# Optimization experiments

Hardware: AMD Instinct MI355X
Metric: run time of the kernel (lower is better)

Reference implementation:

```python
import jax, jax.numpy as jnp
import numpy as np

MAX_LEN = 960
EMB = 200
SQRT_DK = np.sqrt(MAX_LEN).astype(np.float32)  # note: sqrt(max_len), as in source


def setup_inputs() -> dict:
    key = jax.random.key(0)
    k1, k2, k3, k4 = jax.random.split(key, 4)
    B, S, F = 16, 2048, 800
    x = jax.random.normal(k1, (B, S, F), dtype=jnp.float32)
    # torch Linear(960,200) weight init scale ~ 1/sqrt(960); random normal scaled
    scale = 1.0 / np.sqrt(MAX_LEN)
    Wq = jax.random.normal(k2, (MAX_LEN, EMB), dtype=jnp.float32) * scale
    Wk = jax.random.normal(k3, (MAX_LEN, EMB), dtype=jnp.float32) * scale
    Wv = jax.random.normal(k4, (MAX_LEN, EMB), dtype=jnp.float32) * scale
    return {"x": x, "Wq": Wq, "Wk": Wk, "Wv": Wv}


def reference(x, Wq, Wk, Wv):
    # pad feature dim up to MAX_LEN with zeros
    pad = MAX_LEN - x.shape[2]
    x = jnp.pad(x, ((0, 0), (0, 0), (0, pad)))
    gelu = lambda t: jax.nn.gelu(t, approximate=False)  # torch nn.GELU default = exact
    q = gelu(jnp.einsum('bsf,fe->bse', x, Wq))  # [B,S,E]
    k = gelu(jnp.einsum('bsf,fe->bse', x, Wk))
    v = gelu(jnp.einsum('bsf,fe->bse', x, Wv))
    score = jnp.einsum('bqe,bke->bqk', q, k) / SQRT_DK  # [B,S,S]
    attn = jax.nn.softmax(score, axis=-1)
    return jnp.einsum('bqk,bke->bqe', attn, v)  # [B,S,E]
```

## Files before the change

kernel.cpp:

```cpp
#include <hip/hip_runtime.h>
#include <hip/hip_bf16.h>

#define B_  16
#define S_  2048
#define F_  800
#define E_  200
#define EP  224
#define KP  832
#define KSP 256
#define M_  (B_ * S_)

typedef __attribute__((ext_vector_type(8))) short short8;
typedef __attribute__((ext_vector_type(4))) float f32x4;

#define QSCL (0.03227486121839514f * 1.4426950408889634f)

__device__ __forceinline__ unsigned short f2bf(float f) {
    __hip_bfloat16 h = __float2bfloat16(f);
    return *reinterpret_cast<unsigned short*>(&h);
}

__device__ __forceinline__ float exp2_fast(float x) {
    float r;
    asm("v_exp_f32 %0, %1" : "=v"(r) : "v"(x));
    return r;
}

__device__ __forceinline__ float rcp_fast(float x) {
    float r;
    asm("v_rcp_f32 %0, %1" : "=v"(r) : "v"(x));
    return r;
}

__device__ __forceinline__ float gelu_fast(float x) {
    const float i = x + 0.044715f * x * x * x;
    const float z = 2.302265314f * i;
    return x * rcp_fast(1.0f + exp2_fast(-z));
}

__device__ __forceinline__ void gload_lds16(const void* g, void* l) {
    __builtin_amdgcn_global_load_lds(
        (const __attribute__((address_space(1))) unsigned int*)g,
        (__attribute__((address_space(3))) unsigned int*)l, 16, 0, 0);
}

__global__ __launch_bounds__(256)
void prep_x(const float* __restrict__ x, unsigned short* __restrict__ xb) {
    const int id = blockIdx.x * 256 + threadIdx.x;
    const int r  = id / (KP / 8);
    const int c8 = id % (KP / 8);
    ushort4 lo = {0, 0, 0, 0}, hi = {0, 0, 0, 0};
    if (c8 < F_ / 8) {
        const float4 a = *reinterpret_cast<const float4*>(x + (size_t)r * F_ + c8 * 8);
        const float4 b = *reinterpret_cast<const float4*>(x + (size_t)r * F_ + c8 * 8 + 4);
        lo.x = f2bf(a.x); lo.y = f2bf(a.y); lo.z = f2bf(a.z); lo.w = f2bf(a.w);
        hi.x = f2bf(b.x); hi.y = f2bf(b.y); hi.z = f2bf(b.z); hi.w = f2bf(b.w);
    }
    unsigned short* dst = xb + (size_t)r * KP + c8 * 8;
    *reinterpret_cast<ushort4*>(dst) = lo;
    *reinterpret_cast<ushort4*>(dst + 4) = hi;
}

__global__ __launch_bounds__(256)
void prep_w(const float* __restrict__ Wq, const float* __restrict__ Wk,
            const float* __restrict__ Wv, unsigned short* __restrict__ wt) {
    const int id = blockIdx.x * 256 + threadIdx.x;
    const int sel = id / (EP * KP);
    const int rem = id % (EP * KP);
    const int e = rem / KP;
    const int k = rem % KP;
    const float* W = (sel == 0) ? Wq : ((sel == 1) ? Wk : Wv);
    float v = (e < E_ && k < F_) ? W[(size_t)k * E_ + e] : 0.0f;
    wt[id] = f2bf(v);
}

#define STAGE(XB, WB, KK) do {                                                   \
    const int k0s = (KK) * 32;                                                   \
    _Pragma("unroll")                                                            \
    for (int i = 0; i < 2; ++i) {                                                \
        const int j = w * 2 + i;                                                 \
        const int row = 16 * j + rS;                                             \
        gload_lds16(xb + (size_t)(m0 + row) * KP + k0s + ((pS ^ (row & 3)) * 8), \
                    &XB[j * 512]);                                               \
    }                                                                            \
    _Pragma("unroll")                                                            \
    for (int i = 0; i < 4; ++i) {                                                \
        const int j = i * 4 + w;                                                 \
        if (j < 14) {                                                            \
            const int row = 16 * j + rS;                                         \
            gload_lds16(wsel + (size_t)row * KP + k0s + ((pS ^ (row & 3)) * 8),  \
                        &WB[j * 512]);                                           \
        }                                                                        \
    }                                                                            \
} while (0)

#define COMPUTE(XB, WB) do {                                                     \
    short8 afr[4];                                                               \
    _Pragma("unroll")                                                            \
    for (int rf = 0; rf < 4; ++rf) {                                             \
        const int row = wr * 64 + rf * 16 + ln15;                                \
        afr[rf] = *reinterpret_cast<const short8*>(                              \
            &XB[row * 32 + ((g ^ (row & 3)) * 8)]);                              \
    }                                                                            \
    _Pragma("unroll")                                                            \
    for (int cf = 0; cf < 7; ++cf) {                                             \
        const int row = wc * 112 + cf * 16 + ln15;                               \
        short8 bfr = *reinterpret_cast<const short8*>(                           \
            &WB[row * 32 + ((g ^ (row & 3)) * 8)]);                              \
        _Pragma("unroll")                                                        \
        for (int rf = 0; rf < 4; ++rf)                                           \
            acc[rf][cf] = __builtin_amdgcn_mfma_f32_16x16x32_bf16(               \
                afr[rf], bfr, acc[rf][cf], 0, 0, 0);                             \
    }                                                                            \
} while (0)

__global__ __launch_bounds__(256, 2)
void gemm_qkv(const unsigned short* __restrict__ xb,
              const unsigned short* __restrict__ wt,
              unsigned short* __restrict__ qbuf,
              unsigned short* __restrict__ kbuf,
              unsigned short* __restrict__ vtbuf) {
    const int sel = blockIdx.y;
    const int m0 = blockIdx.x * 128;
    const int t = threadIdx.x;
    const int lane = t & 63;
    const int w = t >> 6;
    const int wr = w >> 1;
    const int wc = w & 1;
    const int ln15 = lane & 15;
    const int g = lane >> 4;

    __shared__ __align__(16) unsigned short X0s[128 * 32];
    __shared__ __align__(16) unsigned short W0s[224 * 32];
    __shared__ __align__(16) unsigned short X1s[128 * 32];
    __shared__ __align__(16) unsigned short W1s[224 * 32];

    const unsigned short* wsel = wt + (size_t)sel * EP * KP;

    f32x4 acc[4][7];
#pragma unroll
    for (int i = 0; i < 4; ++i)
#pragma unroll
        for (int j = 0; j < 7; ++j) acc[i][j] = (f32x4)0.0f;

    const int rS = lane >> 2;
    const int pS = lane & 3;

    STAGE(X0s, W0s, 0);
    __syncthreads();
#pragma unroll
    for (int p = 0; p < 12; ++p) {
        STAGE(X1s, W1s, 2 * p + 1);
        COMPUTE(X0s, W0s);
        __syncthreads();
        STAGE(X0s, W0s, 2 * p + 2);
        COMPUTE(X1s, W1s);
        __syncthreads();
    }
    STAGE(X1s, W1s, 25);
    COMPUTE(X0s, W0s);
    __syncthreads();
    COMPUTE(X1s, W1s);

#pragma unroll
    for (int rf = 0; rf < 4; ++rf) {
        const int row = m0 + wr * 64 + rf * 16 + g * 4;
#pragma unroll
        for (int cf = 0; cf < 7; ++cf) {
            const int col = wc * 112 + cf * 16 + ln15;
            if (sel == 0) {
#pragma unroll
                for (int tt = 0; tt < 4; ++tt)
                    qbuf[(size_t)(row + tt) * EP + col] =
                        f2bf(gelu_fast(acc[rf][cf][tt]) * QSCL);
            } else if (sel == 1) {
#pragma unroll
                for (int tt = 0; tt < 4; ++tt)
                    kbuf[(size_t)(row + tt) * KSP + col] = f2bf(gelu_fast(acc[rf][cf][tt]));
            } else {
                const int bb = row >> 11, s = row & 2047;
                ushort4 pk;
                if (col == 200) {
                    pk.x = 0x3F80; pk.y = 0x3F80; pk.z = 0x3F80; pk.w = 0x3F80;
                } else {
                    pk.x = f2bf(gelu_fast(acc[rf][cf][0]));
                    pk.y = f2bf(gelu_fast(acc[rf][cf][1]));
                    pk.z = f2bf(gelu_fast(acc[rf][cf][2]));
                    pk.w = f2bf(gelu_fast(acc[rf][cf][3]));
                }
                *reinterpret_cast<ushort4*>(
                    &vtbuf[((size_t)(bb * EP + col)) * S_ + s]) = pk;
            }
        }
    }
}

#define BQ  128
#define BKV 64

#define ASTAGE(KB, VB, KT) do {                                                  \
    const int kv0s = (KT) * BKV;                                                 \
    {                                                                            \
        const int r_in = lane >> 5;                                              \
        const int p = lane & 31;                                                 \
        _Pragma("unroll")                                                        \
        for (int i = 0; i < 8; ++i) {                                            \
            const int j = w * 8 + i;                                             \
            const int row = 2 * j + r_in;                                        \
            gload_lds16(kb_b + (size_t)(kv0s + row) * KSP + ((p ^ (row & 7)) * 8),\
                        &KB[j * 512]);                                           \
        }                                                                        \
    }                                                                            \
    {                                                                            \
        const int r_in = lane >> 3;                                              \
        const int p = lane & 7;                                                  \
        _Pragma("unroll")                                                        \
        for (int i = 0; i < 7; ++i) {                                            \
            const int j = w * 7 + i;                                             \
            const int row = 8 * j + r_in;                                        \
            gload_lds16(vt_b + (size_t)row * S_ + kv0s + ((p ^ (row & 7)) * 8),  \
                        &VB[j * 512]);                                           \
        }                                                                        \
    }                                                                            \
} while (0)

#define ACOMPUTE(KB, VB) do {                                                    \
    _Pragma("unroll")                                                            \
    for (int rf = 0; rf < 2; ++rf) {                                             \
        f32x4 sacc[4];                                                           \
        _Pragma("unroll")                                                        \
        for (int n = 0; n < 4; ++n) {                                            \
            f32x4 a = (f32x4)0.0f;                                               \
            const int krow = n * 16 + ln15;                                      \
            const unsigned short* kr = &KB[krow * KSP];                          \
            const int rx = krow & 7;                                             \
            _Pragma("unroll")                                                    \
            for (int s = 0; s < 7; ++s) {                                        \
                short8 bf = *reinterpret_cast<const short8*>(                    \
                    kr + (((s * 4 + g) ^ rx) * 8));                              \
                a = __builtin_amdgcn_mfma_f32_16x16x32_bf16(qf[rf][s], bf, a, 0, 0, 0); \
            }                                                                    \
            sacc[n] = a;                                                         \
        }                                                                        \
        _Pragma("unroll")                                                        \
        for (int n = 0; n < 4; ++n)                                              \
            _Pragma("unroll")                                                    \
            for (int tt = 0; tt < 4; ++tt)                                       \
                Plds[w][rf * 16 + g * 4 + tt][n * 16 + ln15] =                   \
                    f2bf(exp2_fast(sacc[n][tt]));                                \
    }                                                                            \
    short8 pf[2][2];                                                             \
    _Pragma("unroll")                                                            \
    for (int rf = 0; rf < 2; ++rf) {                                             \
        pf[rf][0] = *reinterpret_cast<const short8*>(&Plds[w][rf * 16 + ln15][g * 8]); \
        pf[rf][1] = *reinterpret_cast<const short8*>(&Plds[w][rf * 16 + ln15][32 + g * 8]); \
    }                                                                            \
    _Pragma("unroll")                                                            \
    for (int n = 0; n < 14; ++n) {                                               \
        const int vrow = n * 16 + ln15;                                          \
        const unsigned short* vr = &VB[vrow * 64];                               \
        const int rx = vrow & 7;                                                 \
        short8 b0 = *reinterpret_cast<const short8*>(vr + ((g ^ rx) * 8));       \
        short8 b1 = *reinterpret_cast<const short8*>(vr + (((4 + g) ^ rx) * 8)); \
        _Pragma("unroll")                                                        \
        for (int rf = 0; rf < 2; ++rf) {                                         \
            o[rf][n] = __builtin_amdgcn_mfma_f32_16x16x32_bf16(pf[rf][0], b0, o[rf][n], 0, 0, 0); \
            o[rf][n] = __builtin_amdgcn_mfma_f32_16x16x32_bf16(pf[rf][1], b1, o[rf][n], 0, 0, 0); \
        }                                                                        \
    }                                                                            \
} while (0)

__global__ __launch_bounds__(256, 1)
void attn_kernel(const unsigned short* __restrict__ qbuf,
                 const unsigned short* __restrict__ kbuf,
                 const unsigned short* __restrict__ vtbuf,
                 float* __restrict__ out) {
    const int id = blockIdx.x;
    const int slot = id >> 3;
    const int b = 2 * (id & 7) + (slot >> 4);
    const int q0 = (slot & 15) * BQ;
    const int t = threadIdx.x;
    const int lane = t & 63;
    const int w = t >> 6;
    const int ln15 = lane & 15;
    const int g = lane >> 4;

    __shared__ __align__(16) unsigned short Ks[2][BKV * KSP];
    __shared__ __align__(16) unsigned short Vts[2][EP * 64];
    __shared__ __align__(16) unsigned short Plds[4][32][68];

    short8 qf[2][7];
#pragma unroll
    for (int rf = 0; rf < 2; ++rf) {
        const unsigned short* qp =
            qbuf + (size_t)(b * S_ + q0 + w * 32 + rf * 16 + ln15) * EP + g * 8;
#pragma unroll
        for (int s = 0; s < 7; ++s)
            qf[rf][s] = *reinterpret_cast<const short8*>(qp + s * 32);
    }

    f32x4 o[2][14];
#pragma unroll
    for (int rf = 0; rf < 2; ++rf)
#pragma unroll
        for (int i = 0; i < 14; ++i) o[rf][i] = (f32x4)0.0f;

    const unsigned short* kb_b = kbuf + (size_t)b * S_ * KSP;
    const unsigned short* vt_b = vtbuf + (size_t)b * EP * S_;

    ASTAGE(Ks[0], Vts[0], 0);
    __syncthreads();
    for (int kt = 0; kt < S_ / BKV - 1; ++kt) {
        const int cur = kt & 1;
        ASTAGE(Ks[cur ^ 1], Vts[cur ^ 1], kt + 1);
        ACOMPUTE(Ks[cur], Vts[cur]);
        __syncthreads();
    }
    ACOMPUTE(Ks[1], Vts[1]);

#pragma unroll
    for (int rf = 0; rf < 2; ++rf) {
        float l[4];
#pragma unroll
        for (int tt = 0; tt < 4; ++tt)
            l[tt] = __shfl(o[rf][12][tt], (lane & 48) + 8, 64);
#pragma unroll
        for (int tt = 0; tt < 4; ++tt) {
            const float inv = 1.0f / l[tt];
            const int row = q0 + w * 32 + rf * 16 + g * 4 + tt;
            float* op = out + (size_t)(b * S_ + row) * E_;
#pragma unroll
            for (int n = 0; n < 13; ++n) {
                const int e = n * 16 + ln15;
                if (e < E_) op[e] = o[rf][n][tt] * inv;
            }
        }
    }
}

extern "C" void kernel_launch(void* const* d_in, const int* in_sizes, int n_in,
                              void* d_out, int out_size, void* d_ws, size_t ws_size,
                              hipStream_t stream) {
    const float* x  = (const float*)d_in[0];
    const float* Wq = (const float*)d_in[1];
    const float* Wk = (const float*)d_in[2];
    const float* Wv = (const float*)d_in[3];
    float* out = (float*)d_out;

    unsigned short* xb    = (unsigned short*)d_ws;
    unsigned short* wt    = xb + (size_t)M_ * KP;
    unsigned short* qbuf  = wt + (size_t)3 * EP * KP;
    unsigned short* kbuf  = qbuf + (size_t)M_ * EP;
    unsigned short* vtbuf = kbuf + (size_t)M_ * KSP;

    prep_x<<<dim3(M_ * (KP / 8) / 256), 256, 0, stream>>>(x, xb);
    prep_w<<<dim3(3 * EP * KP / 256), 256, 0, stream>>>(Wq, Wk, Wv, wt);
    gemm_qkv<<<dim3(256, 3), 256, 0, stream>>>(xb, wt, qbuf, kbuf, vtbuf);
    attn_kernel<<<dim3(256), 256, 0, stream>>>(qbuf, kbuf, vtbuf, out);
}
```

Measured before the change: 188.4 us.

## Split attention block across 8 waves with 16 query rows each

The attention kernel now launches 512 threads (8 waves) per block instead of 256. Each wave owns 16 query rows rather than 32, which halves the per-wave Q fragments and output accumulators. The K/V staging loads are redistributed across the 8 waves, with a guard for the 28 V chunks. Each K/V tile loaded into LDS is now shared by more waves and register pressure drops, in exchange for the extra cost of synchronising twice as many waves. Launch bounds are raised to (512, 2), but the LDS footprint probably still limits the CU to one block.

```diff
diff --git a/kernel.cpp b/kernel.cpp
--- a/kernel.cpp
+++ b/kernel.cpp
@@ -200,61 +200,55 @@
 
 #define ASTAGE(KB, VB, KT) do {                                                  \
     const int kv0s = (KT) * BKV;                                                 \
-    {                                                                            \
+    {                            \
         const int r_in = lane >> 5;                                              \
         const int p = lane & 31;                                                 \
         _Pragma("unroll")                                                        \
-        for (int i = 0; i < 8; ++i) {                                            \
-            const int j = w * 8 + i;                                             \
+        for (int i = 0; i < 4; ++i) {                                            \
+            const int j = w * 4 + i;                                             \
             const int row = 2 * j + r_in;                                        \
             gload_lds16(kb_b + (size_t)(kv0s + row) * KSP + ((p ^ (row & 7)) * 8),\
                         &KB[j * 512]);                                           \
         }                                                                        \
     }                                                                            \
-    {                                                                            \
+    {                                        \
         const int r_in = lane >> 3;                                              \
         const int p = lane & 7;                                                  \
         _Pragma("unroll")                                                        \
-        for (int i = 0; i < 7; ++i) {                                            \
-            const int j = w * 7 + i;                                             \
-            const int row = 8 * j + r_in;                                        \
-            gload_lds16(vt_b + (size_t)row * S_ + kv0s + ((p ^ (row & 7)) * 8),  \
-                        &VB[j * 512]);                                           \
+        for (int i = 0; i < 4; ++i) {                                            \
+            const int j = i * 8 + w;                                             \
+            if (j < 28) {                                                        \
+                const int row = 8 * j + r_in;                                    \
+                gload_lds16(vt_b + (size_t)row * S_ + kv0s + ((p ^ (row & 7)) * 8),\
+                            &VB[j * 512]);                                       \
+            }                                                                    \
         }                                                                        \
     }                                                                            \
 } while (0)
 
 #define ACOMPUTE(KB, VB) do {                                                    \
-    _Pragma("unroll")                                                            \
-    for (int rf = 0; rf < 2; ++rf) {                                             \
-        f32x4 sacc[4];                                                           \
-        _Pragma("unroll")                                                        \
-        for (int n = 0; n < 4; ++n) {                                            \
-            f32x4 a = (f32x4)0.0f;                                               \
-            const int krow = n * 16 + ln15;                                      \
-            const unsigned short* kr = &KB[krow * KSP];                          \
-            const int rx = krow & 7;                                             \
-            _Pragma("unroll")                                                    \
-            for (int s = 0; s < 7; ++s) {                                        \
-                short8 bf = *reinterpret_cast<const short8*>(                    \
-                    kr + (((s * 4 + g) ^ rx) * 8));                              \
-                a = __builtin_amdgcn_mfma_f32_16x16x32_bf16(qf[rf][s], bf, a, 0, 0, 0); \
-            }                                                                    \
-            sacc[n] = a;                                                         \
+    f32x4 sacc[4];                                                               \
+    _Pragma("unroll")                                                            \
+    for (int n = 0; n < 4; ++n) {                                                \
+        f32x4 a = (f32x4)0.0f;                                                   \
+        const int krow = n * 16 + ln15;                                          \
+        const unsigned short* kr = &KB[krow * KSP];                              \
+        const int rx = krow & 7;                                                 \
+        _Pragma("unroll")                                                        \
+        for (int s = 0; s < 7; ++s) {                                            \
+            short8 bf = *reinterpret_cast<const short8*>(                        \
+                kr + (((s * 4 + g) ^ rx) * 8));                                  \
+            a = __builtin_amdgcn_mfma_f32_16x16x32_bf16(qf[s], bf, a, 0, 0, 0);  \
         }                                                                        \
-        _Pragma("unroll")                                                        \
-        for (int n = 0; n < 4; ++n)                                              \
-            _Pragma("unroll")                                                    \
-            for (int tt = 0; tt < 4; ++tt)                                       \
-                Plds[w][rf * 16 + g * 4 + tt][n * 16 + ln15] =                   \
-                    f2bf(exp2_fast(sacc[n][tt]));                                \
-    }                                                                            \
-    short8 pf[2][2];                                                             \
-    _Pragma("unroll")                                                            \
-    for (int rf = 0; rf < 2; ++rf) {                                             \
-        pf[rf][0] = *reinterpret_cast<const short8*>(&Plds[w][rf * 16 + ln15][g * 8]); \
-        pf[rf][1] = *reinterpret_cast<const short8*>(&Plds[w][rf * 16 + ln15][32 + g * 8]); \
-    }                                                                            \
+        sacc[n] = a;                                                             \
+    }                                                                            \
+    _Pragma("unroll")                                                            \
+    for (int n = 0; n < 4; ++n)                                                  \
+        _Pragma("unroll")                                                        \
+        for (int tt = 0; tt < 4; ++tt)                                           \
+            Plds[w][g * 4 + tt][n * 16 + ln15] = f2bf(exp2_fast(sacc[n][tt]));   \
+    short8 pf0 = *reinterpret_cast<const short8*>(&Plds[w][ln15][g * 8]);        \
+    short8 pf1 = *reinterpret_cast<const short8*>(&Plds[w][ln15][32 + g * 8]);   \
     _Pragma("unroll")                                                            \
     for (int n = 0; n < 14; ++n) {                                               \
         const int vrow = n * 16 + ln15;                                          \
@@ -262,15 +256,12 @@
         const int rx = vrow & 7;                                                 \
         short8 b0 = *reinterpret_cast<const short8*>(vr + ((g ^ rx) * 8));       \
         short8 b1 = *reinterpret_cast<const short8*>(vr + (((4 + g) ^ rx) * 8)); \
-        _Pragma("unroll")                                                        \
-        for (int rf = 0; rf < 2; ++rf) {                                         \
-            o[rf][n] = __builtin_amdgcn_mfma_f32_16x16x32_bf16(pf[rf][0], b0, o[rf][n], 0, 0, 0); \
-            o[rf][n] = __builtin_amdgcn_mfma_f32_16x16x32_bf16(pf[rf][1], b1, o[rf][n], 0, 0, 0); \
-        }                                                                        \
+        o[n] = __builtin_amdgcn_mfma_f32_16x16x32_bf16(pf0, b0, o[n], 0, 0, 0);  \
+        o[n] = __builtin_amdgcn_mfma_f32_16x16x32_bf16(pf1, b1, o[n], 0, 0, 0);  \
     }                                                                            \
 } while (0)
 
-__global__ __launch_bounds__(256, 1)
+__global__ __launch_bounds__(512, 2)
 void attn_kernel(const unsigned short* __restrict__ qbuf,
                  const unsigned short* __restrict__ kbuf,
                  const unsigned short* __restrict__ vtbuf,
@@ -287,23 +278,20 @@
 
     __shared__ __align__(16) unsigned short Ks[2][BKV * KSP];
     __shared__ __align__(16) unsigned short Vts[2][EP * 64];
-    __shared__ __align__(16) unsigned short Plds[4][32][68];
-
-    short8 qf[2][7];
-#pragma unroll
-    for (int rf = 0; rf < 2; ++rf) {
+    __shared__ __align__(16) unsigned short Plds[8][16][68];
+
+    short8 qf[7];
+    {
         const unsigned short* qp =
-            qbuf + (size_t)(b * S_ + q0 + w * 32 + rf * 16 + ln15) * EP + g * 8;
+            qbuf + (size_t)(b * S_ + q0 + w * 16 + ln15) * EP + g * 8;
 #pragma unroll
         for (int s = 0; s < 7; ++s)
-            qf[rf][s] = *reinterpret_cast<const short8*>(qp + s * 32);
-    }
-
-    f32x4 o[2][14];
-#pragma unroll
-    for (int rf = 0; rf < 2; ++rf)
-#pragma unroll
-        for (int i = 0; i < 14; ++i) o[rf][i] = (f32x4)0.0f;
+            qf[s] = *reinterpret_cast<const short8*>(qp + s * 32);
+    }
+
+    f32x4 o[14];
+#pragma unroll
+    for (int i = 0; i < 14; ++i) o[i] = (f32x4)0.0f;
 
     const unsigned short* kb_b = kbuf + (size_t)b * S_ * KSP;
     const unsigned short* vt_b = vtbuf + (size_t)b * EP * S_;
@@ -318,21 +306,20 @@
     }
     ACOMPUTE(Ks[1], Vts[1]);
 
-#pragma unroll
-    for (int rf = 0; rf < 2; ++rf) {
+    {
         float l[4];
 #pragma unroll
         for (int tt = 0; tt < 4; ++tt)
-            l[tt] = __shfl(o[rf][12][tt], (lane & 48) + 8, 64);
+            l[tt] = __shfl(o[12][tt], (lane & 48) + 8, 64);
 #pragma unroll
         for (int tt = 0; tt < 4; ++tt) {
             const float inv = 1.0f / l[tt];
-            const int row = q0 + w * 32 + rf * 16 + g * 4 + tt;
+            const int row = q0 + w * 16 + g * 4 + tt;
             float* op = out + (size_t)(b * S_ + row) * E_;
 #pragma unroll
             for (int n = 0; n < 13; ++n) {
                 const int e = n * 16 + ln15;
-                if (e < E_) op[e] = o[rf][n][tt] * inv;
+                if (e < E_) op[e] = o[n][tt] * inv;
             }
         }
     }
@@ -356,5 +343,5 @@
     prep_x<<<dim3(M_ * (KP / 8) / 256), 256, 0, stream>>>(x, xb);
     prep_w<<<dim3(3 * EP * KP / 256), 256, 0, stream>>>(Wq, Wk, Wv, wt);
     gemm_qkv<<<dim3(256, 3), 256, 0, stream>>>(xb, wt, qbuf, kbuf, vtbuf);
-    attn_kernel<<<dim3(256), 256, 0, stream>>>(qbuf, kbuf, vtbuf, out);
-}
+    attn_kernel<<<dim3(256), 512, 0, stream>>>(qbuf, kbuf, vtbuf, out);
+}
```

Result: faster. 170.0 us (-9.8%).

## Split attention output dim across two blocks and compute denominator via MFMA ones

Applied to the files above, without the earlier changes.

The attention kernel now splits the 224-wide value/output dimension into two halves handled by separate blocks, doubling the grid to 512 blocks so more CUs have work. The KV tile shrinks to 32 and the softmax denominator is accumulated with an MFMA against a ones vector instead of being read from the padded ones column. The cost is that QK^T and exp are recomputed in both halves, roughly doubling score work, while the smaller per-block working set and LDS footprint may improve occupancy and load balance.

```diff
diff --git a/kernel.cpp b/kernel.cpp
--- a/kernel.cpp
+++ b/kernel.cpp
@@ -196,40 +196,44 @@
 }
 
 #define BQ  128
-#define BKV 64
+#define BKV 32
 
 #define ASTAGE(KB, VB, KT) do {                                                  \
     const int kv0s = (KT) * BKV;                                                 \
-    {                                                                            \
+    {              \
         const int r_in = lane >> 5;                                              \
         const int p = lane & 31;                                                 \
         _Pragma("unroll")                                                        \
-        for (int i = 0; i < 8; ++i) {                                            \
-            const int j = w * 8 + i;                                             \
+        for (int i = 0; i < 4; ++i) {                                            \
+            const int j = w * 4 + i;                                             \
             const int row = 2 * j + r_in;                                        \
             gload_lds16(kb_b + (size_t)(kv0s + row) * KSP + ((p ^ (row & 7)) * 8),\
                         &KB[j * 512]);                                           \
         }                                                                        \
     }                                                                            \
-    {                                                                            \
-        const int r_in = lane >> 3;                                              \
-        const int p = lane & 7;                                                  \
-        _Pragma("unroll")                                                        \
-        for (int i = 0; i < 7; ++i) {                                            \
-            const int j = w * 7 + i;                                             \
-            const int row = 8 * j + r_in;                                        \
-            gload_lds16(vt_b + (size_t)row * S_ + kv0s + ((p ^ (row & 7)) * 8),  \
-                        &VB[j * 512]);                                           \
+    {             \
+        const int r_in = lane >> 2;                                              \
+        const int p = lane & 3;                                                  \
+        _Pragma("unroll")                                                        \
+        for (int i = 0; i < 2; ++i) {                                            \
+            const int j = i * 4 + w;                                             \
+            if (j < 7) {                                                         \
+                const int lr = 16 * j + r_in;                                    \
+                gload_lds16(vt_b + (size_t)(ehBase + lr) * S_ + kv0s +           \
+                                ((p ^ (lr & 3)) * 8),                            \
+                            &VB[j * 512]);                                       \
+            }                                                                    \
         }                                                                        \
     }                                                                            \
 } while (0)
 
 #define ACOMPUTE(KB, VB) do {                                                    \
+    short8 pf[2];                                                                \
     _Pragma("unroll")                                                            \
     for (int rf = 0; rf < 2; ++rf) {                                             \
-        f32x4 sacc[4];                                                           \
-        _Pragma("unroll")                                                        \
-        for (int n = 0; n < 4; ++n) {                                            \
+        f32x4 sacc[2];                                                           \
+        _Pragma("unroll")                                                        \
+        for (int n = 0; n < 2; ++n) {                                            \
             f32x4 a = (f32x4)0.0f;                                               \
             const int krow = n * 16 + ln15;                                      \
             const unsigned short* kr = &KB[krow * KSP];                          \
@@ -243,30 +247,22 @@
             sacc[n] = a;                                                         \
         }                                                                        \
         _Pragma("unroll")                                                        \
-        for (int n = 0; n < 4; ++n)                                              \
+        for (int n = 0; n < 2; ++n)                                              \
             _Pragma("unroll")                                                    \
             for (int tt = 0; tt < 4; ++tt)                                       \
                 Plds[w][rf * 16 + g * 4 + tt][n * 16 + ln15] =                   \
                     f2bf(exp2_fast(sacc[n][tt]));                                \
-    }                                                                            \
-    short8 pf[2][2];                                                             \
-    _Pragma("unroll")                                                            \
-    for (int rf = 0; rf < 2; ++rf) {                                             \
-        pf[rf][0] = *reinterpret_cast<const short8*>(&Plds[w][rf * 16 + ln15][g * 8]); \
-        pf[rf][1] = *reinterpret_cast<const short8*>(&Plds[w][rf * 16 + ln15][32 + g * 8]); \
-    }                                                                            \
-    _Pragma("unroll")                                                            \
-    for (int n = 0; n < 14; ++n) {                                               \
-        const int vrow = n * 16 + ln15;                                          \
-        const unsigned short* vr = &VB[vrow * 64];                               \
-        const int rx = vrow & 7;                                                 \
-        short8 b0 = *reinterpret_cast<const short8*>(vr + ((g ^ rx) * 8));       \
-        short8 b1 = *reinterpret_cast<const short8*>(vr + (((4 + g) ^ rx) * 8)); \
-        _Pragma("unroll")                                                        \
-        for (int rf = 0; rf < 2; ++rf) {                                         \
-            o[rf][n] = __builtin_amdgcn_mfma_f32_16x16x32_bf16(pf[rf][0], b0, o[rf][n], 0, 0, 0); \
-            o[rf][n] = __builtin_amdgcn_mfma_f32_16x16x32_bf16(pf[rf][1], b1, o[rf][n], 0, 0, 0); \
-        }                                                                        \
+        pf[rf] = *reinterpret_cast<const short8*>(&Plds[w][rf * 16 + ln15][g * 8]); \
+        dn[rf] = __builtin_amdgcn_mfma_f32_16x16x32_bf16(pf[rf], ones8, dn[rf], 0, 0, 0); \
+    }                                                                            \
+    _Pragma("unroll")                                                            \
+    for (int n = 0; n < 7; ++n) {                                                \
+        const int lr = n * 16 + ln15;                                            \
+        short8 b0 = *reinterpret_cast<const short8*>(                            \
+            &VB[lr * 32 + ((g ^ (lr & 3)) * 8)]);                                \
+        _Pragma("unroll")                                                        \
+        for (int rf = 0; rf < 2; ++rf)                                           \
+            o[rf][n] = __builtin_amdgcn_mfma_f32_16x16x32_bf16(pf[rf], b0, o[rf][n], 0, 0, 0); \
     }                                                                            \
 } while (0)
 
@@ -277,8 +273,11 @@
                  float* __restrict__ out) {
     const int id = blockIdx.x;
     const int slot = id >> 3;
-    const int b = 2 * (id & 7) + (slot >> 4);
-    const int q0 = (slot & 15) * BQ;
+    const int eh = slot & 1;
+    const int rest = slot >> 1;
+    const int b = 2 * (id & 7) + (rest >> 4);
+    const int q0 = (rest & 15) * BQ;
+    const int ehBase = eh * 112;
     const int t = threadIdx.x;
     const int lane = t & 63;
     const int w = t >> 6;
@@ -286,8 +285,16 @@
     const int g = lane >> 4;
 
     __shared__ __align__(16) unsigned short Ks[2][BKV * KSP];
-    __shared__ __align__(16) unsigned short Vts[2][EP * 64];
-    __shared__ __align__(16) unsigned short Plds[4][32][68];
+    __shared__ __align__(16) unsigned short Vts[2][112 * BKV];
+    __shared__ __align__(16) unsigned short Plds[4][32][48];
+
+    short8 ones8;
+    {
+        union { unsigned short u[8]; short8 s; } ou;
+#pragma unroll
+        for (int i = 0; i < 8; ++i) ou.u[i] = 0x3F80;
+        ones8 = ou.s;
+    }
 
     short8 qf[2][7];
 #pragma unroll
@@ -299,11 +306,14 @@
             qf[rf][s] = *reinterpret_cast<const short8*>(qp + s * 32);
     }
 
-    f32x4 o[2][14];
-#pragma unroll
-    for (int rf = 0; rf < 2; ++rf)
-#pragma unroll
-        for (int i = 0; i < 14; ++i) o[rf][i] = (f32x4)0.0f;
+    f32x4 o[2][7];
+    f32x4 dn[2];
+#pragma unroll
+    for (int rf = 0; rf < 2; ++rf) {
+        dn[rf] = (f32x4)0.0f;
+#pragma unroll
+        for (int i = 0; i < 7; ++i) o[rf][i] = (f32x4)0.0f;
+    }
 
     const unsigned short* kb_b = kbuf + (size_t)b * S_ * KSP;
     const unsigned short* vt_b = vtbuf + (size_t)b * EP * S_;
@@ -320,18 +330,14 @@
 
 #pragma unroll
     for (int rf = 0; rf < 2; ++rf) {
-        float l[4];
-#pragma unroll
-        for (int tt = 0; tt < 4; ++tt)
-            l[tt] = __shfl(o[rf][12][tt], (lane & 48) + 8, 64);
 #pragma unroll
         for (int tt = 0; tt < 4; ++tt) {
-            const float inv = 1.0f / l[tt];
+            const float inv = 1.0f / dn[rf][tt];
             const int row = q0 + w * 32 + rf * 16 + g * 4 + tt;
             float* op = out + (size_t)(b * S_ + row) * E_;
 #pragma unroll
-            for (int n = 0; n < 13; ++n) {
-                const int e = n * 16 + ln15;
+            for (int n = 0; n < 7; ++n) {
+                const int e = ehBase + n * 16 + ln15;
                 if (e < E_) op[e] = o[rf][n][tt] * inv;
             }
         }
@@ -356,5 +362,5 @@
     prep_x<<<dim3(M_ * (KP / 8) / 256), 256, 0, stream>>>(x, xb);
     prep_w<<<dim3(3 * EP * KP / 256), 256, 0, stream>>>(Wq, Wk, Wv, wt);
     gemm_qkv<<<dim3(256, 3), 256, 0, stream>>>(xb, wt, qbuf, kbuf, vtbuf);
-    attn_kernel<<<dim3(256), 256, 0, stream>>>(qbuf, kbuf, vtbuf, out);
-}
+    attn_kernel<<<dim3(512), 256, 0, stream>>>(qbuf, kbuf, vtbuf, out);
+}
```

Measured after the change: 189.1 us. Within noise of the previous version (+0.3%).
